# Optimization experiments

Measured on AMD Instinct MI355X. Metric: run time of the kernel, lower is better.

## Reference

```python
import jax, jax.numpy as jnp
import numpy as np

N_NODES = 50000
N_EDGES = 640000
IN_C, HID_C, OUT_C = 64, 128, 64


def _glorot(key, fan_in, fan_out):
    lim = float(np.sqrt(6.0 / (fan_in + fan_out)))
    return jax.random.uniform(key, (fan_in, fan_out), jnp.float32, -lim, lim)


def setup_inputs() -> dict:
    key = jax.random.key(0)
    ks = jax.random.split(key, 16)
    x = jax.random.normal(ks[0], (N_NODES, IN_C), jnp.float32)
    edge_index = jax.random.randint(ks[1], (2, N_EDGES), 0, N_NODES, jnp.int64)
    # SAGEConv params: out = mean_aggr(x_j) @ Wl + x @ Wr + b
    dims = [(IN_C, HID_C), (HID_C, HID_C), (HID_C, OUT_C)]
    params = {}
    for i, (fi, fo) in enumerate(dims):
        params[f"Wl{i}"] = _glorot(ks[2 + 3 * i], fi, fo)
        params[f"Wr{i}"] = _glorot(ks[3 + 3 * i], fi, fo)
        params[f"b{i}"] = jnp.zeros((fo,), jnp.float32)
    # classifier: Linear(64,32) -> ReLU -> Linear(32,1) -> Sigmoid (dropout off in eval)
    params["Wc1"] = _glorot(ks[11], OUT_C, 32)
    params["bc1"] = jnp.zeros((32,), jnp.float32)
    params["Wc2"] = _glorot(ks[12], 32, 1)
    params["bc2"] = jnp.zeros((1,), jnp.float32)
    return {"x": x, "edge_index": edge_index, **params}


def _sage_conv(x, src, dst, Wl, Wr, b):
    # gather neighbor (source) features along edges, mean-aggregate at target
    msgs = x[src]                                                    # [E, C]
    agg = jax.ops.segment_sum(msgs, dst, num_segments=N_NODES)      # [N, C]
    deg = jax.ops.segment_sum(jnp.ones((src.shape[0], 1), x.dtype), dst,
                              num_segments=N_NODES)                 # [N, 1]
    agg = agg / jnp.maximum(deg, 1.0)
    return agg @ Wl + x @ Wr + b


def reference(x, edge_index, Wl0, Wr0, b0, Wl1, Wr1, b1, Wl2, Wr2, b2,
              Wc1, bc1, Wc2, bc2):
    src, dst = edge_index[0], edge_index[1]
    h = jax.nn.relu(_sage_conv(x, src, dst, Wl0, Wr0, b0))
    h = jax.nn.relu(_sage_conv(h, src, dst, Wl1, Wr1, b1))
    h = _sage_conv(h, src, dst, Wl2, Wr2, b2)                       # [N, 64]
    h = jax.nn.relu(h @ Wc1 + bc1)                                  # [N, 32]
    return jax.nn.sigmoid(h @ Wc2 + bc2)                            # [N, 1]
```

## Files before the change

### kernel.cpp

```cpp
#include <hip/hip_runtime.h>
#include <math.h>

#define NN 50000
#define NE 640000
#define CAP 64

typedef short short8 __attribute__((ext_vector_type(8)));
typedef float f32x4  __attribute__((ext_vector_type(4)));

__device__ __forceinline__ unsigned bfr(float f) {
    unsigned u = __float_as_uint(f);
    return (u + 0x7FFFu + ((u >> 16) & 1u)) >> 16;
}
__device__ __forceinline__ unsigned pk2(float a, float b) { return bfr(a) | (bfr(b) << 16); }
__device__ __forceinline__ float bflo(unsigned u) { return __uint_as_float(u << 16); }
__device__ __forceinline__ float bfhi(unsigned u) { return __uint_as_float(u & 0xFFFF0000u); }

__device__ __forceinline__ void packOne(const float* Wl, const float* Wr,
                                        unsigned short* wp, int idx,
                                        int CIN, int COUT) {
    int k = idx / COUT, n = idx % COUT;
    float v = (k < CIN) ? Wl[k * COUT + n] : Wr[(k - CIN) * COUT + n];
    int kt = k >> 5, quad = (k >> 3) & 3, j = k & 7;
    int nt = n >> 4, l16 = n & 15;
    int NT = COUT / 16;
    wp[(((kt * NT + nt) * 64) + quad * 16 + l16) * 8 + j] = (unsigned short)bfr(v);
}

__global__ __launch_bounds__(256) void
k_prep(const int* __restrict__ src, const int* __restrict__ dst,
       int* __restrict__ cnt, int* __restrict__ nbr,
       const float* __restrict__ x, unsigned* __restrict__ xb,
       const float* Wl0, const float* Wr0, const float* Wl1, const float* Wr1,
       const float* Wl2, const float* Wr2, const float* Wc1,
       unsigned short* wp0, unsigned short* wp1, unsigned short* wp2,
       unsigned short* wpc) {
    const int b = blockIdx.x, t = threadIdx.x;
    if (b < 2500) {
        int e = b * 256 + t;
        if (e < NE) {
            int d = dst[e];
            int p = atomicAdd(&cnt[d], 1);
            if (p < CAP) nbr[d * CAP + p] = src[e];
        }
    } else if (b < 5625) {
        int i = (b - 2500) * 256 + t;
        if (i < NN * 16) {
            float4 v = ((const float4*)x)[i];
            ((uint2*)xb)[i] = make_uint2(pk2(v.x, v.y), pk2(v.z, v.w));
        }
    } else {
        int idx = (b - 5625) * 256 + t;
        if (idx < 16384) {
            packOne(Wl0, Wr0, wp0, idx, 64, 128);
        } else if (idx < 49152) {
            packOne(Wl1, Wr1, wp1, idx - 16384, 128, 128);
        } else if (idx < 65536) {
            packOne(Wl2, Wr2, wp2, idx - 49152, 128, 64);
        } else if (idx < 67584) {
            packOne(Wc1, Wc1, wpc, idx - 65536, 64, 32);
        }
    }
}

template <int LOGC>
__global__ __launch_bounds__(256) void
k_aggregate(const unsigned* __restrict__ xu, const int* __restrict__ nbr,
            const int* __restrict__ cnt, unsigned* __restrict__ aggu, int N) {
    constexpr int RU = 1 << (LOGC - 1);
    constexpr int PC = RU / 16;
    const int gw   = (blockIdx.x * 256 + threadIdx.x) >> 6;
    const int lane = threadIdx.x & 63;
    const int qw = lane >> 4, l16 = lane & 15;
    if (gw >= N) return;
    const int deg = cnt[gw];
    const int m = (deg < CAP) ? deg : CAP;

    int idx = 0;
    if (lane < m) idx = nbr[gw * CAP + lane];

    float a[2 * PC] = {};

#pragma unroll 4
    for (int j = 0; j < m; j += 4) {
        const int n = __shfl(idx, (j + qw) & 63);
        const bool valid = (j + qw) < m;
        if (PC == 2) {
            const uint2 u = *(const uint2*)(xu + (size_t)n * RU + l16 * 2);
            if (valid) {
                a[0] += bflo(u.x); a[1] += bfhi(u.x);
                a[2] += bflo(u.y); a[3] += bfhi(u.y);
            }
        } else {
            const uint4 u = *(const uint4*)(xu + (size_t)n * RU + l16 * 4);
            if (valid) {
                a[0] += bflo(u.x); a[1] += bfhi(u.x);
                a[2] += bflo(u.y); a[3] += bfhi(u.y);
                a[4] += bflo(u.z); a[5] += bfhi(u.z);
                a[6] += bflo(u.w); a[7] += bfhi(u.w);
            }
        }
    }

#pragma unroll
    for (int c = 0; c < 2 * PC; ++c) {
        a[c] += __shfl_xor(a[c], 16);
        a[c] += __shfl_xor(a[c], 32);
    }

    if (qw == 0) {
        const float di = 1.0f / (float)((deg > 1) ? deg : 1);
        if (PC == 2) {
            uint2 o = make_uint2(pk2(a[0] * di, a[1] * di), pk2(a[2] * di, a[3] * di));
            *(uint2*)(aggu + (size_t)gw * RU + l16 * 2) = o;
        } else {
            uint4 o = make_uint4(pk2(a[0] * di, a[1] * di), pk2(a[2] * di, a[3] * di),
                                 pk2(a[4] * di, a[5] * di), pk2(a[6] * di, a[7] * di));
            *(uint4*)(aggu + (size_t)gw * RU + l16 * 4) = o;
        }
    }
}

template <int CIN, int COUT, bool RELU>
__global__ __launch_bounds__(256) void
k_mfma(const unsigned short* __restrict__ Agg, const unsigned short* __restrict__ X,
       const unsigned short* __restrict__ Wpack, const float* __restrict__ bias,
       unsigned short* __restrict__ outp, int N) {
    constexpr int KT = (2 * CIN) / 32;
    constexpr int NT = COUT / 16;

    __shared__ short Bs[KT * NT * 64 * 8];

    const int t = threadIdx.x;
    const int wave = t >> 6, lane = t & 63;
    const int quad = lane >> 4, l16 = lane & 15;

    constexpr int NCHUNK = KT * NT * 64;
    for (int i = t; i < NCHUNK; i += 256)
        *(uint4*)&Bs[i * 8] = ((const uint4*)Wpack)[i];
    __syncthreads();

    const int row_base = blockIdx.x * 128 + wave * 32;
    int r0 = row_base + l16;      if (r0 >= N) r0 = N - 1;
    int r1 = row_base + 16 + l16; if (r1 >= N) r1 = N - 1;

    f32x4 acc[2][NT] = {};

    for (int kt = 0; kt < KT; ++kt) {
        const unsigned short* P = (kt < KT / 2) ? Agg : X;
        const int kb = (kt < KT / 2) ? kt * 32 : kt * 32 - CIN;
        const short8 a0 = *(const short8*)(P + (size_t)r0 * CIN + kb + quad * 8);
        const short8 a1 = *(const short8*)(P + (size_t)r1 * CIN + kb + quad * 8);
#pragma unroll
        for (int nt = 0; nt < NT; ++nt) {
            const short8 bfrag = *(const short8*)&Bs[((kt * NT + nt) * 64 + lane) * 8];
            acc[0][nt] = __builtin_amdgcn_mfma_f32_16x16x32_bf16(a0, bfrag, acc[0][nt], 0, 0, 0);
            acc[1][nt] = __builtin_amdgcn_mfma_f32_16x16x32_bf16(a1, bfrag, acc[1][nt], 0, 0, 0);
        }
    }

#pragma unroll
    for (int nt = 0; nt < NT; ++nt) {
        const int col = nt * 16 + l16;
        const float bb = bias[col];
#pragma unroll
        for (int s = 0; s < 2; ++s) {
#pragma unroll
            for (int rg = 0; rg < 4; ++rg) {
                int row = row_base + s * 16 + quad * 4 + rg;
                if (row < N) {
                    float v = acc[s][nt][rg] + bb;
                    if (RELU) v = fmaxf(v, 0.f);
                    outp[(size_t)row * COUT + col] = (unsigned short)bfr(v);
                }
            }
        }
    }
}

__global__ __launch_bounds__(256) void
k_mfma_cls(const unsigned short* __restrict__ Agg, const unsigned short* __restrict__ X,
           const unsigned short* __restrict__ Wpack, const unsigned short* __restrict__ WpackC,
           const float* __restrict__ bias, const float* __restrict__ bc1,
           const float* __restrict__ Wc2, const float* __restrict__ bc2,
           float* __restrict__ out, int N) {
    constexpr int CIN = 128, COUT = 64;
    constexpr int KT = 8, NT = 4;

    __shared__ __align__(16) short Bs[KT * NT * 64 * 8];
    __shared__ __align__(16) short Wc1s[2 * 2 * 64 * 8];
    __shared__ __align__(16) short Hs[8 * 16 * 64];
    __shared__ float sW2[32], sbc1[32];

    const int t = threadIdx.x;
    const int wave = t >> 6, lane = t & 63;
    const int quad = lane >> 4, l16 = lane & 15;

    for (int i = t; i < KT * NT * 64; i += 256)
        *(uint4*)&Bs[i * 8] = ((const uint4*)Wpack)[i];
    if (t < 256) *(uint4*)&Wc1s[t * 8] = ((const uint4*)WpackC)[t];
    if (t < 32) { sW2[t] = Wc2[t]; sbc1[t] = bc1[t]; }
    __syncthreads();

    const int row_base = blockIdx.x * 128 + wave * 32;
    int r0 = row_base + l16;      if (r0 >= N) r0 = N - 1;
    int r1 = row_base + 16 + l16; if (r1 >= N) r1 = N - 1;

    f32x4 acc[2][NT] = {};

    for (int kt = 0; kt < KT; ++kt) {
        const unsigned short* P = (kt < KT / 2) ? Agg : X;
        const int kb = (kt < KT / 2) ? kt * 32 : kt * 32 - CIN;
        const short8 a0 = *(const short8*)(P + (size_t)r0 * CIN + kb + quad * 8);
        const short8 a1 = *(const short8*)(P + (size_t)r1 * CIN + kb + quad * 8);
#pragma unroll
        for (int nt = 0; nt < NT; ++nt) {
            const short8 bfrag = *(const short8*)&Bs[((kt * NT + nt) * 64 + lane) * 8];
            acc[0][nt] = __builtin_amdgcn_mfma_f32_16x16x32_bf16(a0, bfrag, acc[0][nt], 0, 0, 0);
            acc[1][nt] = __builtin_amdgcn_mfma_f32_16x16x32_bf16(a1, bfrag, acc[1][nt], 0, 0, 0);
        }
    }

#pragma unroll
    for (int nt = 0; nt < NT; ++nt) {
        const float bb = bias[nt * 16 + l16];
#pragma unroll
        for (int s = 0; s < 2; ++s)
#pragma unroll
            for (int rg = 0; rg < 4; ++rg)
                Hs[(wave * 2 + s) * 1024 + (quad * 4 + rg) * 64 + nt * 16 + l16] =
                    (unsigned short)bfr(acc[s][nt][rg] + bb);
    }
    __syncthreads();

    f32x4 sacc[2][2] = {};
#pragma unroll
    for (int s = 0; s < 2; ++s)
#pragma unroll
        for (int kt2 = 0; kt2 < 2; ++kt2) {
            const short8 af = *(const short8*)&Hs[(wave * 2 + s) * 1024 + l16 * 64 +
                                                  kt2 * 32 + quad * 8];
#pragma unroll
            for (int nt2 = 0; nt2 < 2; ++nt2) {
                const short8 bf = *(const short8*)&Wc1s[((kt2 * 2 + nt2) * 64 + lane) * 8];
                sacc[s][nt2] = __builtin_amdgcn_mfma_f32_16x16x32_bf16(af, bf, sacc[s][nt2], 0, 0, 0);
            }
        }

    const float b1a = sbc1[l16], b1b = sbc1[16 + l16];
    const float w2a = sW2[l16],  w2b = sW2[16 + l16];
    const float b2v = bc2[0];
#pragma unroll
    for (int s = 0; s < 2; ++s)
#pragma unroll
        for (int rg = 0; rg < 4; ++rg) {
            float p = fmaxf(sacc[s][0][rg] + b1a, 0.f) * w2a +
                      fmaxf(sacc[s][1][rg] + b1b, 0.f) * w2b;
#pragma unroll
            for (int off = 1; off < 16; off <<= 1) p += __shfl_xor(p, off);
            if (l16 == 0) {
                int row = row_base + s * 16 + quad * 4 + rg;
                if (row < N) out[row] = 1.0f / (1.0f + expf(-(p + b2v)));
            }
        }
}

extern "C" void kernel_launch(void* const* d_in, const int* in_sizes, int n_in,
                              void* d_out, int out_size, void* d_ws, size_t ws_size,
                              hipStream_t stream) {
    const float* x   = (const float*)d_in[0];
    const int*   ei  = (const int*)d_in[1];
    const int*   src = ei;
    const int*   dst = ei + NE;
    const float* Wl0 = (const float*)d_in[2];
    const float* Wr0 = (const float*)d_in[3];
    const float* b0  = (const float*)d_in[4];
    const float* Wl1 = (const float*)d_in[5];
    const float* Wr1 = (const float*)d_in[6];
    const float* b1  = (const float*)d_in[7];
    const float* Wl2 = (const float*)d_in[8];
    const float* Wr2 = (const float*)d_in[9];
    const float* b2  = (const float*)d_in[10];
    const float* Wc1 = (const float*)d_in[11];
    const float* bc1 = (const float*)d_in[12];
    const float* Wc2 = (const float*)d_in[13];
    const float* bc2 = (const float*)d_in[14];
    float* out = (float*)d_out;

    char*  ws   = (char*)d_ws;
    int*   cnt  = (int*)(ws);
    unsigned short* wp0 = (unsigned short*)(ws + (size_t)256 * 1024);
    unsigned short* wp1 = (unsigned short*)(ws + (size_t)352 * 1024);
    unsigned short* wp2 = (unsigned short*)(ws + (size_t)448 * 1024);
    unsigned short* wpc = (unsigned short*)(ws + (size_t)512 * 1024);
    int*   nbr  = (int*)(ws + (size_t)1 * (1 << 20));
    unsigned short* xb   = (unsigned short*)(ws + (size_t)16 * (1 << 20));
    unsigned short* aggb = (unsigned short*)(ws + (size_t)24 * (1 << 20));
    unsigned short* h0b  = (unsigned short*)(ws + (size_t)40 * (1 << 20));
    unsigned short* h1b  = (unsigned short*)(ws + (size_t)56 * (1 << 20));

    const int B = 256;
    const int AGG_GRID = (NN + 3) / 4;
    const int MFMA_GRID = (NN + 127) / 128;

    hipMemsetAsync(cnt, 0, (size_t)NN * sizeof(int), stream);
    k_prep<<<5889, B, 0, stream>>>(src, dst, cnt, nbr, x, (unsigned*)xb,
                                   Wl0, Wr0, Wl1, Wr1, Wl2, Wr2, Wc1,
                                   wp0, wp1, wp2, wpc);

    k_aggregate<6><<<AGG_GRID, B, 0, stream>>>((const unsigned*)xb, nbr, cnt,
                                               (unsigned*)aggb, NN);
    k_mfma<64, 128, true><<<MFMA_GRID, 256, 0, stream>>>(aggb, xb, wp0, b0, h0b, NN);

    k_aggregate<7><<<AGG_GRID, B, 0, stream>>>((const unsigned*)h0b, nbr, cnt,
                                               (unsigned*)aggb, NN);
    k_mfma<128, 128, true><<<MFMA_GRID, 256, 0, stream>>>(aggb, h0b, wp1, b1, h1b, NN);

    k_aggregate<7><<<AGG_GRID, B, 0, stream>>>((const unsigned*)h1b, nbr, cnt,
                                               (unsigned*)aggb, NN);
    k_mfma_cls<<<MFMA_GRID, 256, 0, stream>>>(aggb, h1b, wp2, wpc, b2, bc1, Wc2, bc2,
                                              out, NN);
}
```

Baseline: 239.3 us.

## Fuse neighbor aggregation into per-layer MFMA kernels via LDS staging

Each SAGE layer is now a single kernel: every block gathers and mean-aggregates neighbor features for its 128 nodes into a padded LDS tile, then runs the MFMA GEMM, reading the aggregated half from LDS and the self half from global memory. This removes three aggregate launches and the global write and reread of the aggregated buffer. Weight fragments are now read straight from global or L2 instead of being staged in LDS. The cost is much less parallelism in the gather: 391 blocks, each wave walking 32 nodes one after another, where before one wave handled one node. This risks exposing latency on a memory-bound gather.

```diff
diff --git a/kernel.cpp b/kernel.cpp
--- a/kernel.cpp
+++ b/kernel.cpp
@@ -63,97 +63,112 @@
     }
 }
 
-template <int LOGC>
-__global__ __launch_bounds__(256) void
-k_aggregate(const unsigned* __restrict__ xu, const int* __restrict__ nbr,
-            const int* __restrict__ cnt, unsigned* __restrict__ aggu, int N) {
-    constexpr int RU = 1 << (LOGC - 1);
-    constexpr int PC = RU / 16;
-    const int gw   = (blockIdx.x * 256 + threadIdx.x) >> 6;
-    const int lane = threadIdx.x & 63;
-    const int qw = lane >> 4, l16 = lane & 15;
-    if (gw >= N) return;
-    const int deg = cnt[gw];
-    const int m = (deg < CAP) ? deg : CAP;
-
-    int idx = 0;
-    if (lane < m) idx = nbr[gw * CAP + lane];
-
-    float a[2 * PC] = {};
-
+template <int CIN, int RPAD>
+__device__ __forceinline__ void
+gather_to_lds(short* As, const unsigned short* __restrict__ Xprev,
+              const int* __restrict__ nbr, const int* __restrict__ cnt,
+              int nb0, int N, int wave, int lane, int qw, int l16) {
+    constexpr int PC = CIN / 32;
+    const unsigned* xu = (const unsigned*)Xprev;
+
+    int node = nb0 + wave * 32; if (node >= N) node = N - 1;
+    int dcur = cnt[node];
+    int scur = nbr[node * CAP + lane];
+
+    for (int it = 0; it < 32; ++it) {
+        const int deg = dcur;
+        const int sl  = scur;
+        if (it + 1 < 32) {
+            int nn = nb0 + wave * 32 + it + 1; if (nn >= N) nn = N - 1;
+            dcur = cnt[nn];
+            scur = nbr[nn * CAP + lane];
+        }
+        const int m = (deg < CAP) ? deg : CAP;
+        const int sc = (lane < m) ? sl : 0;
+
+        float a[2 * PC] = {};
 #pragma unroll 4
-    for (int j = 0; j < m; j += 4) {
-        const int n = __shfl(idx, (j + qw) & 63);
-        const bool valid = (j + qw) < m;
-        if (PC == 2) {
-            const uint2 u = *(const uint2*)(xu + (size_t)n * RU + l16 * 2);
-            if (valid) {
-                a[0] += bflo(u.x); a[1] += bfhi(u.x);
-                a[2] += bflo(u.y); a[3] += bfhi(u.y);
-            }
-        } else {
-            const uint4 u = *(const uint4*)(xu + (size_t)n * RU + l16 * 4);
-            if (valid) {
-                a[0] += bflo(u.x); a[1] += bfhi(u.x);
-                a[2] += bflo(u.y); a[3] += bfhi(u.y);
-                a[4] += bflo(u.z); a[5] += bfhi(u.z);
-                a[6] += bflo(u.w); a[7] += bfhi(u.w);
-            }
-        }
-    }
-
-#pragma unroll
-    for (int c = 0; c < 2 * PC; ++c) {
-        a[c] += __shfl_xor(a[c], 16);
-        a[c] += __shfl_xor(a[c], 32);
-    }
-
-    if (qw == 0) {
-        const float di = 1.0f / (float)((deg > 1) ? deg : 1);
-        if (PC == 2) {
-            uint2 o = make_uint2(pk2(a[0] * di, a[1] * di), pk2(a[2] * di, a[3] * di));
-            *(uint2*)(aggu + (size_t)gw * RU + l16 * 2) = o;
-        } else {
-            uint4 o = make_uint4(pk2(a[0] * di, a[1] * di), pk2(a[2] * di, a[3] * di),
-                                 pk2(a[4] * di, a[5] * di), pk2(a[6] * di, a[7] * di));
-            *(uint4*)(aggu + (size_t)gw * RU + l16 * 4) = o;
+        for (int j = 0; j < m; j += 4) {
+            const int n = __shfl(sc, (j + qw) & 63);
+            const bool valid = (j + qw) < m;
+            if (PC == 2) {
+                const uint2 u = *(const uint2*)(xu + (size_t)n * 32 + l16 * 2);
+                if (valid) {
+                    a[0] += bflo(u.x); a[1] += bfhi(u.x);
+                    a[2] += bflo(u.y); a[3] += bfhi(u.y);
+                }
+            } else {
+                const uint4 u = *(const uint4*)(xu + (size_t)n * 64 + l16 * 4);
+                if (valid) {
+                    a[0] += bflo(u.x); a[1] += bfhi(u.x);
+                    a[2] += bflo(u.y); a[3] += bfhi(u.y);
+                    a[4] += bflo(u.z); a[5] += bfhi(u.z);
+                    a[6] += bflo(u.w); a[7] += bfhi(u.w);
+                }
+            }
+        }
+
+#pragma unroll
+        for (int c = 0; c < 2 * PC; ++c) {
+            a[c] += __shfl_xor(a[c], 16);
+            a[c] += __shfl_xor(a[c], 32);
+        }
+
+        if (qw == 0) {
+            const float di = 1.0f / (float)((deg > 1) ? deg : 1);
+            const int row = wave * 32 + it;
+            if (PC == 2) {
+                uint2 o = make_uint2(pk2(a[0] * di, a[1] * di), pk2(a[2] * di, a[3] * di));
+                *(uint2*)&As[row * RPAD + l16 * 4] = o;
+            } else {
+                uint4 o = make_uint4(pk2(a[0] * di, a[1] * di), pk2(a[2] * di, a[3] * di),
+                                     pk2(a[4] * di, a[5] * di), pk2(a[6] * di, a[7] * di));
+                *(uint4*)&As[row * RPAD + l16 * 8] = o;
+            }
         }
     }
 }
 
 template <int CIN, int COUT, bool RELU>
-__global__ __launch_bounds__(256) void
-k_mfma(const unsigned short* __restrict__ Agg, const unsigned short* __restrict__ X,
-       const unsigned short* __restrict__ Wpack, const float* __restrict__ bias,
-       unsigned short* __restrict__ outp, int N) {
+__global__ __launch_bounds__(256, 2) void
+k_layer(const unsigned short* __restrict__ Xprev, const int* __restrict__ nbr,
+        const int* __restrict__ cnt, const unsigned short* __restrict__ Wpack,
+        const float* __restrict__ bias, unsigned short* __restrict__ outp, int N) {
     constexpr int KT = (2 * CIN) / 32;
     constexpr int NT = COUT / 16;
-
-    __shared__ short Bs[KT * NT * 64 * 8];
-
-    const int t = threadIdx.x;
-    const int wave = t >> 6, lane = t & 63;
-    const int quad = lane >> 4, l16 = lane & 15;
-
-    constexpr int NCHUNK = KT * NT * 64;
-    for (int i = t; i < NCHUNK; i += 256)
-        *(uint4*)&Bs[i * 8] = ((const uint4*)Wpack)[i];
+    constexpr int RPAD = CIN + 10;
+
+    __shared__ __align__(16) short As[128 * RPAD];
+
+    const int t = threadIdx.x, wave = t >> 6, lane = t & 63;
+    const int qw = lane >> 4, l16 = lane & 15;
+    const int nb0 = blockIdx.x * 128;
+
+    gather_to_lds<CIN, RPAD>(As, Xprev, nbr, cnt, nb0, N, wave, lane, qw, l16);
     __syncthreads();
 
-    const int row_base = blockIdx.x * 128 + wave * 32;
-    int r0 = row_base + l16;      if (r0 >= N) r0 = N - 1;
-    int r1 = row_base + 16 + l16; if (r1 >= N) r1 = N - 1;
+    const int row_base = nb0 + wave * 32;
+    int r0g = row_base + l16;      if (r0g >= N) r0g = N - 1;
+    int r1g = row_base + 16 + l16; if (r1g >= N) r1g = N - 1;
+    const int l0 = wave * 32 + l16;
+    const int l1 = wave * 32 + 16 + l16;
 
     f32x4 acc[2][NT] = {};
 
     for (int kt = 0; kt < KT; ++kt) {
-        const unsigned short* P = (kt < KT / 2) ? Agg : X;
-        const int kb = (kt < KT / 2) ? kt * 32 : kt * 32 - CIN;
-        const short8 a0 = *(const short8*)(P + (size_t)r0 * CIN + kb + quad * 8);
-        const short8 a1 = *(const short8*)(P + (size_t)r1 * CIN + kb + quad * 8);
+        short8 a0, a1;
+        if (kt < KT / 2) {
+            const int kb = kt * 32 + qw * 8;
+            a0 = *(const short8*)&As[l0 * RPAD + kb];
+            a1 = *(const short8*)&As[l1 * RPAD + kb];
+        } else {
+            const int kb = kt * 32 - CIN + qw * 8;
+            a0 = *(const short8*)(Xprev + (size_t)r0g * CIN + kb);
+            a1 = *(const short8*)(Xprev + (size_t)r1g * CIN + kb);
+        }
 #pragma unroll
         for (int nt = 0; nt < NT; ++nt) {
-            const short8 bfrag = *(const short8*)&Bs[((kt * NT + nt) * 64 + lane) * 8];
+            const short8 bfrag = *(const short8*)(Wpack + (size_t)((kt * NT + nt) * 64 + lane) * 8);
             acc[0][nt] = __builtin_amdgcn_mfma_f32_16x16x32_bf16(a0, bfrag, acc[0][nt], 0, 0, 0);
             acc[1][nt] = __builtin_amdgcn_mfma_f32_16x16x32_bf16(a1, bfrag, acc[1][nt], 0, 0, 0);
         }
@@ -167,7 +182,7 @@
         for (int s = 0; s < 2; ++s) {
 #pragma unroll
             for (int rg = 0; rg < 4; ++rg) {
-                int row = row_base + s * 16 + quad * 4 + rg;
+                int row = row_base + s * 16 + qw * 4 + rg;
                 if (row < N) {
                     float v = acc[s][nt][rg] + bb;
                     if (RELU) v = fmaxf(v, 0.f);
@@ -178,44 +193,48 @@
     }
 }
 
-__global__ __launch_bounds__(256) void
-k_mfma_cls(const unsigned short* __restrict__ Agg, const unsigned short* __restrict__ X,
-           const unsigned short* __restrict__ Wpack, const unsigned short* __restrict__ WpackC,
-           const float* __restrict__ bias, const float* __restrict__ bc1,
-           const float* __restrict__ Wc2, const float* __restrict__ bc2,
-           float* __restrict__ out, int N) {
+__global__ __launch_bounds__(256, 2) void
+k_layer_cls(const unsigned short* __restrict__ Xprev, const int* __restrict__ nbr,
+            const int* __restrict__ cnt, const unsigned short* __restrict__ Wpack,
+            const unsigned short* __restrict__ WpackC, const float* __restrict__ bias,
+            const float* __restrict__ bc1, const float* __restrict__ Wc2,
+            const float* __restrict__ bc2, float* __restrict__ out, int N) {
     constexpr int CIN = 128, COUT = 64;
     constexpr int KT = 8, NT = 4;
-
-    __shared__ __align__(16) short Bs[KT * NT * 64 * 8];
-    __shared__ __align__(16) short Wc1s[2 * 2 * 64 * 8];
+    constexpr int RPAD = CIN + 10;
+
+    __shared__ __align__(16) short As[128 * RPAD];
     __shared__ __align__(16) short Hs[8 * 16 * 64];
-    __shared__ float sW2[32], sbc1[32];
-
-    const int t = threadIdx.x;
-    const int wave = t >> 6, lane = t & 63;
-    const int quad = lane >> 4, l16 = lane & 15;
-
-    for (int i = t; i < KT * NT * 64; i += 256)
-        *(uint4*)&Bs[i * 8] = ((const uint4*)Wpack)[i];
-    if (t < 256) *(uint4*)&Wc1s[t * 8] = ((const uint4*)WpackC)[t];
-    if (t < 32) { sW2[t] = Wc2[t]; sbc1[t] = bc1[t]; }
+
+    const int t = threadIdx.x, wave = t >> 6, lane = t & 63;
+    const int qw = lane >> 4, l16 = lane & 15;
+    const int nb0 = blockIdx.x * 128;
+
+    gather_to_lds<CIN, RPAD>(As, Xprev, nbr, cnt, nb0, N, wave, lane, qw, l16);
     __syncthreads();
 
-    const int row_base = blockIdx.x * 128 + wave * 32;
-    int r0 = row_base + l16;      if (r0 >= N) r0 = N - 1;
-    int r1 = row_base + 16 + l16; if (r1 >= N) r1 = N - 1;
+    const int row_base = nb0 + wave * 32;
+    int r0g = row_base + l16;      if (r0g >= N) r0g = N - 1;
+    int r1g = row_base + 16 + l16; if (r1g >= N) r1g = N - 1;
+    const int l0 = wave * 32 + l16;
+    const int l1 = wave * 32 + 16 + l16;
 
     f32x4 acc[2][NT] = {};
 
     for (int kt = 0; kt < KT; ++kt) {
-        const unsigned short* P = (kt < KT / 2) ? Agg : X;
-        const int kb = (kt < KT / 2) ? kt * 32 : kt * 32 - CIN;
-        const short8 a0 = *(const short8*)(P + (size_t)r0 * CIN + kb + quad * 8);
-        const short8 a1 = *(const short8*)(P + (size_t)r1 * CIN + kb + quad * 8);
+        short8 a0, a1;
+        if (kt < KT / 2) {
+            const int kb = kt * 32 + qw * 8;
+            a0 = *(const short8*)&As[l0 * RPAD + kb];
+            a1 = *(const short8*)&As[l1 * RPAD + kb];
+        } else {
+            const int kb = kt * 32 - CIN + qw * 8;
+            a0 = *(const short8*)(Xprev + (size_t)r0g * CIN + kb);
+            a1 = *(const short8*)(Xprev + (size_t)r1g * CIN + kb);
+        }
 #pragma unroll
         for (int nt = 0; nt < NT; ++nt) {
-            const short8 bfrag = *(const short8*)&Bs[((kt * NT + nt) * 64 + lane) * 8];
+            const short8 bfrag = *(const short8*)(Wpack + (size_t)((kt * NT + nt) * 64 + lane) * 8);
             acc[0][nt] = __builtin_amdgcn_mfma_f32_16x16x32_bf16(a0, bfrag, acc[0][nt], 0, 0, 0);
             acc[1][nt] = __builtin_amdgcn_mfma_f32_16x16x32_bf16(a1, bfrag, acc[1][nt], 0, 0, 0);
         }
@@ -228,7 +247,7 @@
         for (int s = 0; s < 2; ++s)
 #pragma unroll
             for (int rg = 0; rg < 4; ++rg)
-                Hs[(wave * 2 + s) * 1024 + (quad * 4 + rg) * 64 + nt * 16 + l16] =
+                Hs[(wave * 2 + s) * 1024 + (qw * 4 + rg) * 64 + nt * 16 + l16] =
                     (unsigned short)bfr(acc[s][nt][rg] + bb);
     }
     __syncthreads();
@@ -239,16 +258,16 @@
 #pragma unroll
         for (int kt2 = 0; kt2 < 2; ++kt2) {
             const short8 af = *(const short8*)&Hs[(wave * 2 + s) * 1024 + l16 * 64 +
-                                                  kt2 * 32 + quad * 8];
+                                                  kt2 * 32 + qw * 8];
 #pragma unroll
             for (int nt2 = 0; nt2 < 2; ++nt2) {
-                const short8 bf = *(const short8*)&Wc1s[((kt2 * 2 + nt2) * 64 + lane) * 8];
+                const short8 bf = *(const short8*)(WpackC + (size_t)((kt2 * 2 + nt2) * 64 + lane) * 8);
                 sacc[s][nt2] = __builtin_amdgcn_mfma_f32_16x16x32_bf16(af, bf, sacc[s][nt2], 0, 0, 0);
             }
         }
 
-    const float b1a = sbc1[l16], b1b = sbc1[16 + l16];
-    const float w2a = sW2[l16],  w2b = sW2[16 + l16];
+    const float b1a = bc1[l16], b1b = bc1[16 + l16];
+    const float w2a = Wc2[l16], w2b = Wc2[16 + l16];
     const float b2v = bc2[0];
 #pragma unroll
     for (int s = 0; s < 2; ++s)
@@ -259,7 +278,7 @@
 #pragma unroll
             for (int off = 1; off < 16; off <<= 1) p += __shfl_xor(p, off);
             if (l16 == 0) {
-                int row = row_base + s * 16 + quad * 4 + rg;
+                int row = row_base + s * 16 + qw * 4 + rg;
                 if (row < N) out[row] = 1.0f / (1.0f + expf(-(p + b2v)));
             }
         }
@@ -294,30 +313,20 @@
     unsigned short* wp2 = (unsigned short*)(ws + (size_t)448 * 1024);
     unsigned short* wpc = (unsigned short*)(ws + (size_t)512 * 1024);
     int*   nbr  = (int*)(ws + (size_t)1 * (1 << 20));
-    unsigned short* xb   = (unsigned short*)(ws + (size_t)16 * (1 << 20));
-    unsigned short* aggb = (unsigned short*)(ws + (size_t)24 * (1 << 20));
-    unsigned short* h0b  = (unsigned short*)(ws + (size_t)40 * (1 << 20));
-    unsigned short* h1b  = (unsigned short*)(ws + (size_t)56 * (1 << 20));
+    unsigned short* xb  = (unsigned short*)(ws + (size_t)16 * (1 << 20));
+    unsigned short* h0b = (unsigned short*)(ws + (size_t)24 * (1 << 20));
+    unsigned short* h1b = (unsigned short*)(ws + (size_t)40 * (1 << 20));
 
     const int B = 256;
-    const int AGG_GRID = (NN + 3) / 4;
-    const int MFMA_GRID = (NN + 127) / 128;
+    const int LAYER_GRID = (NN + 127) / 128;
 
     hipMemsetAsync(cnt, 0, (size_t)NN * sizeof(int), stream);
     k_prep<<<5889, B, 0, stream>>>(src, dst, cnt, nbr, x, (unsigned*)xb,
                                    Wl0, Wr0, Wl1, Wr1, Wl2, Wr2, Wc1,
                                    wp0, wp1, wp2, wpc);
 
-    k_aggregate<6><<<AGG_GRID, B, 0, stream>>>((const unsigned*)xb, nbr, cnt,
-                                               (unsigned*)aggb, NN);
-    k_mfma<64, 128, true><<<MFMA_GRID, 256, 0, stream>>>(aggb, xb, wp0, b0, h0b, NN);
-
-    k_aggregate<7><<<AGG_GRID, B, 0, stream>>>((const unsigned*)h0b, nbr, cnt,
-                                               (unsigned*)aggb, NN);
-    k_mfma<128, 128, true><<<MFMA_GRID, 256, 0, stream>>>(aggb, h0b, wp1, b1, h1b, NN);
-
-    k_aggregate<7><<<AGG_GRID, B, 0, stream>>>((const unsigned*)h1b, nbr, cnt,
-                                               (unsigned*)aggb, NN);
-    k_mfma_cls<<<MFMA_GRID, 256, 0, stream>>>(aggb, h1b, wp2, wpc, b2, bc1, Wc2, bc2,
+    k_layer<64, 128, true><<<LAYER_GRID, B, 0, stream>>>(xb, nbr, cnt, wp0, b0, h0b, NN);
+    k_layer<128, 128, true><<<LAYER_GRID, B, 0, stream>>>(h0b, nbr, cnt, wp1, b1, h1b, NN);
+    k_layer_cls<<<LAYER_GRID, B, 0, stream>>>(h1b, nbr, cnt, wp2, wpc, b2, bc1, Wc2, bc2,
                                               out, NN);
 }
```

New measurement: 339.9 us. 1.42x slower.

## Fuse all GNN stages into one persistent cooperative kernel with grid syncs

Applied to the files above, without the earlier changes.

Replaces the seven separate launches (prep, three aggregate and three MFMA stages) with a single persistent cooperative kernel that grid-strides over work and uses grid.sync between phases. The aim is to remove per-launch overhead and the tail gaps between dependent kernels. The weights are now read from global memory instead of being staged in LDS, both in the fused kernel and in the fallback kernels. The fused path also caps the grid at 2048 blocks, which limits how much parallelism the aggregation phases can use, and each grid.sync adds its own cost.

```diff
diff --git a/kernel.cpp b/kernel.cpp
--- a/kernel.cpp
+++ b/kernel.cpp
@@ -1,5 +1,8 @@
 #include <hip/hip_runtime.h>
+#include <hip/hip_cooperative_groups.h>
 #include <math.h>
+
+namespace cg = cooperative_groups;
 
 #define NN 50000
 #define NE 640000
@@ -25,6 +28,240 @@
     int nt = n >> 4, l16 = n & 15;
     int NT = COUT / 16;
     wp[(((kt * NT + nt) * 64) + quad * 16 + l16) * 8 + j] = (unsigned short)bfr(v);
+}
+
+template <int LOGC>
+__device__ __forceinline__ void
+agg_phase(const unsigned* __restrict__ xu, const int* __restrict__ nbr,
+          const int* __restrict__ cnt, unsigned* __restrict__ aggu,
+          int wgl, int nwave, int lane) {
+    constexpr int RU = 1 << (LOGC - 1);
+    constexpr int PC = RU / 16;
+    const int qw = lane >> 4, l16 = lane & 15;
+
+    for (int gw = wgl; gw < NN; gw += nwave) {
+        const int deg = cnt[gw];
+        const int m = (deg < CAP) ? deg : CAP;
+
+        int idx = 0;
+        if (lane < m) idx = nbr[gw * CAP + lane];
+
+        float a[2 * PC] = {};
+
+#pragma unroll 4
+        for (int j = 0; j < m; j += 4) {
+            const int n = __shfl(idx, (j + qw) & 63);
+            const bool valid = (j + qw) < m;
+            if (PC == 2) {
+                const uint2 u = *(const uint2*)(xu + (size_t)n * RU + l16 * 2);
+                if (valid) {
+                    a[0] += bflo(u.x); a[1] += bfhi(u.x);
+                    a[2] += bflo(u.y); a[3] += bfhi(u.y);
+                }
+            } else {
+                const uint4 u = *(const uint4*)(xu + (size_t)n * RU + l16 * 4);
+                if (valid) {
+                    a[0] += bflo(u.x); a[1] += bfhi(u.x);
+                    a[2] += bflo(u.y); a[3] += bfhi(u.y);
+                    a[4] += bflo(u.z); a[5] += bfhi(u.z);
+                    a[6] += bflo(u.w); a[7] += bfhi(u.w);
+                }
+            }
+        }
+
+#pragma unroll
+        for (int c = 0; c < 2 * PC; ++c) {
+            a[c] += __shfl_xor(a[c], 16);
+            a[c] += __shfl_xor(a[c], 32);
+        }
+
+        if (qw == 0) {
+            const float di = 1.0f / (float)((deg > 1) ? deg : 1);
+            if (PC == 2) {
+                uint2 o = make_uint2(pk2(a[0] * di, a[1] * di), pk2(a[2] * di, a[3] * di));
+                *(uint2*)(aggu + (size_t)gw * RU + l16 * 2) = o;
+            } else {
+                uint4 o = make_uint4(pk2(a[0] * di, a[1] * di), pk2(a[2] * di, a[3] * di),
+                                     pk2(a[4] * di, a[5] * di), pk2(a[6] * di, a[7] * di));
+                *(uint4*)(aggu + (size_t)gw * RU + l16 * 4) = o;
+            }
+        }
+    }
+}
+
+template <int CIN, int COUT, bool RELU>
+__device__ __forceinline__ void
+mfma_phase(const unsigned short* __restrict__ Agg, const unsigned short* __restrict__ X,
+           const unsigned short* __restrict__ Wpack, const float* __restrict__ bias,
+           unsigned short* __restrict__ outp, int blk, int gstride, int wave, int lane) {
+    constexpr int KT = (2 * CIN) / 32;
+    constexpr int NT = COUT / 16;
+    const int quad = lane >> 4, l16 = lane & 15;
+    const int NTILE = (NN + 127) / 128;
+
+    for (int tile = blk; tile < NTILE; tile += gstride) {
+        const int row_base = tile * 128 + wave * 32;
+        int r0 = row_base + l16;      if (r0 >= NN) r0 = NN - 1;
+        int r1 = row_base + 16 + l16; if (r1 >= NN) r1 = NN - 1;
+
+        f32x4 acc[2][NT] = {};
+
+        for (int kt = 0; kt < KT; ++kt) {
+            const unsigned short* P = (kt < KT / 2) ? Agg : X;
+            const int kb = (kt < KT / 2) ? kt * 32 : kt * 32 - CIN;
+            const short8 a0 = *(const short8*)(P + (size_t)r0 * CIN + kb + quad * 8);
+            const short8 a1 = *(const short8*)(P + (size_t)r1 * CIN + kb + quad * 8);
+#pragma unroll
+            for (int nt = 0; nt < NT; ++nt) {
+                const short8 bfrag = *(const short8*)(Wpack + (size_t)((kt * NT + nt) * 64 + lane) * 8);
+                acc[0][nt] = __builtin_amdgcn_mfma_f32_16x16x32_bf16(a0, bfrag, acc[0][nt], 0, 0, 0);
+                acc[1][nt] = __builtin_amdgcn_mfma_f32_16x16x32_bf16(a1, bfrag, acc[1][nt], 0, 0, 0);
+            }
+        }
+
+#pragma unroll
+        for (int nt = 0; nt < NT; ++nt) {
+            const int col = nt * 16 + l16;
+            const float bb = bias[col];
+#pragma unroll
+            for (int s = 0; s < 2; ++s) {
+#pragma unroll
+                for (int rg = 0; rg < 4; ++rg) {
+                    int row = row_base + s * 16 + quad * 4 + rg;
+                    if (row < NN) {
+                        float v = acc[s][nt][rg] + bb;
+                        if (RELU) v = fmaxf(v, 0.f);
+                        outp[(size_t)row * COUT + col] = (unsigned short)bfr(v);
+                    }
+                }
+            }
+        }
+    }
+}
+
+__global__ __launch_bounds__(256) void
+k_all(const int* __restrict__ src, const int* __restrict__ dst,
+      const float* __restrict__ x,
+      const float* Wl0, const float* Wr0, const float* b0,
+      const float* Wl1, const float* Wr1, const float* b1,
+      const float* Wl2, const float* Wr2, const float* b2,
+      const float* Wc1, const float* bc1, const float* Wc2, const float* bc2,
+      int* cnt, int* nbr, unsigned short* xb,
+      unsigned short* wp0, unsigned short* wp1, unsigned short* wp2,
+      unsigned short* wpc,
+      unsigned short* aggb, unsigned short* h0b, unsigned short* h1b,
+      float* out) {
+    cg::grid_group grid = cg::this_grid();
+
+    __shared__ __align__(16) short Hs[8 * 16 * 64];
+
+    const int t = threadIdx.x, b = blockIdx.x;
+    const int nthr = gridDim.x * 256;
+    const int nwave = nthr >> 6;
+    const int gt = b * 256 + t;
+    const int wave = t >> 6, lane = t & 63;
+    const int wgl = gt >> 6;
+    const int quad = lane >> 4, l16 = lane & 15;
+
+    for (int e = gt; e < NE; e += nthr) {
+        int d = dst[e];
+        int p = atomicAdd(&cnt[d], 1);
+        if (p < CAP) nbr[d * CAP + p] = src[e];
+    }
+    for (int i = gt; i < NN * 16; i += nthr) {
+        float4 v = ((const float4*)x)[i];
+        ((uint2*)xb)[i] = make_uint2(pk2(v.x, v.y), pk2(v.z, v.w));
+    }
+    for (int i = gt; i < 67584; i += nthr) {
+        if (i < 16384) packOne(Wl0, Wr0, wp0, i, 64, 128);
+        else if (i < 49152) packOne(Wl1, Wr1, wp1, i - 16384, 128, 128);
+        else if (i < 65536) packOne(Wl2, Wr2, wp2, i - 49152, 128, 64);
+        else packOne(Wc1, Wc1, wpc, i - 65536, 64, 32);
+    }
+    grid.sync();
+
+    agg_phase<6>((const unsigned*)xb, nbr, cnt, (unsigned*)aggb, wgl, nwave, lane);
+    grid.sync();
+    mfma_phase<64, 128, true>(aggb, xb, wp0, b0, h0b, b, gridDim.x, wave, lane);
+    grid.sync();
+
+    agg_phase<7>((const unsigned*)h0b, nbr, cnt, (unsigned*)aggb, wgl, nwave, lane);
+    grid.sync();
+    mfma_phase<128, 128, true>(aggb, h0b, wp1, b1, h1b, b, gridDim.x, wave, lane);
+    grid.sync();
+
+    agg_phase<7>((const unsigned*)h1b, nbr, cnt, (unsigned*)aggb, wgl, nwave, lane);
+    grid.sync();
+
+    {
+        constexpr int CIN = 128, NT = 4, KT = 8;
+        const int NTILE = (NN + 127) / 128;
+
+        for (int tile = b; tile < NTILE; tile += gridDim.x) {
+            const int row_base = tile * 128 + wave * 32;
+            int r0 = row_base + l16;      if (r0 >= NN) r0 = NN - 1;
+            int r1 = row_base + 16 + l16; if (r1 >= NN) r1 = NN - 1;
+
+            f32x4 acc[2][NT] = {};
+
+            for (int kt = 0; kt < KT; ++kt) {
+                const unsigned short* P = (kt < KT / 2) ? aggb : h1b;
+                const int kb = (kt < KT / 2) ? kt * 32 : kt * 32 - CIN;
+                const short8 a0 = *(const short8*)(P + (size_t)r0 * CIN + kb + quad * 8);
+                const short8 a1 = *(const short8*)(P + (size_t)r1 * CIN + kb + quad * 8);
+#pragma unroll
+                for (int nt = 0; nt < NT; ++nt) {
+                    const short8 bfrag = *(const short8*)(wp2 + (size_t)((kt * NT + nt) * 64 + lane) * 8);
+                    acc[0][nt] = __builtin_amdgcn_mfma_f32_16x16x32_bf16(a0, bfrag, acc[0][nt], 0, 0, 0);
+                    acc[1][nt] = __builtin_amdgcn_mfma_f32_16x16x32_bf16(a1, bfrag, acc[1][nt], 0, 0, 0);
+                }
+            }
+
+#pragma unroll
+            for (int nt = 0; nt < NT; ++nt) {
+                const float bb = b2[nt * 16 + l16];
+#pragma unroll
+                for (int s = 0; s < 2; ++s)
+#pragma unroll
+                    for (int rg = 0; rg < 4; ++rg)
+                        Hs[(wave * 2 + s) * 1024 + (quad * 4 + rg) * 64 + nt * 16 + l16] =
+                            (unsigned short)bfr(acc[s][nt][rg] + bb);
+            }
+            __syncthreads();
+
+            f32x4 sacc[2][2] = {};
+#pragma unroll
+            for (int s = 0; s < 2; ++s)
+#pragma unroll
+                for (int kt2 = 0; kt2 < 2; ++kt2) {
+                    const short8 af = *(const short8*)&Hs[(wave * 2 + s) * 1024 + l16 * 64 +
+                                                          kt2 * 32 + quad * 8];
+#pragma unroll
+                    for (int nt2 = 0; nt2 < 2; ++nt2) {
+                        const short8 bf = *(const short8*)(wpc + (size_t)((kt2 * 2 + nt2) * 64 + lane) * 8);
+                        sacc[s][nt2] = __builtin_amdgcn_mfma_f32_16x16x32_bf16(af, bf, sacc[s][nt2], 0, 0, 0);
+                    }
+                }
+
+            const float b1a = bc1[l16], b1b = bc1[16 + l16];
+            const float w2a = Wc2[l16], w2b = Wc2[16 + l16];
+            const float b2v = bc2[0];
+#pragma unroll
+            for (int s = 0; s < 2; ++s)
+#pragma unroll
+                for (int rg = 0; rg < 4; ++rg) {
+                    float p = fmaxf(sacc[s][0][rg] + b1a, 0.f) * w2a +
+                              fmaxf(sacc[s][1][rg] + b1b, 0.f) * w2b;
+#pragma unroll
+                    for (int off = 1; off < 16; off <<= 1) p += __shfl_xor(p, off);
+                    if (l16 == 0) {
+                        int row = row_base + s * 16 + quad * 4 + rg;
+                        if (row < NN) out[row] = 1.0f / (1.0f + expf(-(p + b2v)));
+                    }
+                }
+            __syncthreads();
+        }
+    }
 }
 
 __global__ __launch_bounds__(256) void
@@ -51,15 +288,10 @@
         }
     } else {
         int idx = (b - 5625) * 256 + t;
-        if (idx < 16384) {
-            packOne(Wl0, Wr0, wp0, idx, 64, 128);
-        } else if (idx < 49152) {
-            packOne(Wl1, Wr1, wp1, idx - 16384, 128, 128);
-        } else if (idx < 65536) {
-            packOne(Wl2, Wr2, wp2, idx - 49152, 128, 64);
-        } else if (idx < 67584) {
-            packOne(Wc1, Wc1, wpc, idx - 65536, 64, 32);
-        }
+        if (idx < 16384) packOne(Wl0, Wr0, wp0, idx, 64, 128);
+        else if (idx < 49152) packOne(Wl1, Wr1, wp1, idx - 16384, 128, 128);
+        else if (idx < 65536) packOne(Wl2, Wr2, wp2, idx - 49152, 128, 64);
+        else if (idx < 67584) packOne(Wc1, Wc1, wpc, idx - 65536, 64, 32);
     }
 }
 
@@ -67,58 +299,9 @@
 __global__ __launch_bounds__(256) void
 k_aggregate(const unsigned* __restrict__ xu, const int* __restrict__ nbr,
             const int* __restrict__ cnt, unsigned* __restrict__ aggu, int N) {
-    constexpr int RU = 1 << (LOGC - 1);
-    constexpr int PC = RU / 16;
-    const int gw   = (blockIdx.x * 256 + threadIdx.x) >> 6;
-    const int lane = threadIdx.x & 63;
-    const int qw = lane >> 4, l16 = lane & 15;
-    if (gw >= N) return;
-    const int deg = cnt[gw];
-    const int m = (deg < CAP) ? deg : CAP;
-
-    int idx = 0;
-    if (lane < m) idx = nbr[gw * CAP + lane];
-
-    float a[2 * PC] = {};
-
-#pragma unroll 4
-    for (int j = 0; j < m; j += 4) {
-        const int n = __shfl(idx, (j + qw) & 63);
-        const bool valid = (j + qw) < m;
-        if (PC == 2) {
-            const uint2 u = *(const uint2*)(xu + (size_t)n * RU + l16 * 2);
-            if (valid) {
-                a[0] += bflo(u.x); a[1] += bfhi(u.x);
-                a[2] += bflo(u.y); a[3] += bfhi(u.y);
-            }
-        } else {
-            const uint4 u = *(const uint4*)(xu + (size_t)n * RU + l16 * 4);
-            if (valid) {
-                a[0] += bflo(u.x); a[1] += bfhi(u.x);
-                a[2] += bflo(u.y); a[3] += bfhi(u.y);
-                a[4] += bflo(u.z); a[5] += bfhi(u.z);
-                a[6] += bflo(u.w); a[7] += bfhi(u.w);
-            }
-        }
-    }
-
-#pragma unroll
-    for (int c = 0; c < 2 * PC; ++c) {
-        a[c] += __shfl_xor(a[c], 16);
-        a[c] += __shfl_xor(a[c], 32);
-    }
-
-    if (qw == 0) {
-        const float di = 1.0f / (float)((deg > 1) ? deg : 1);
-        if (PC == 2) {
-            uint2 o = make_uint2(pk2(a[0] * di, a[1] * di), pk2(a[2] * di, a[3] * di));
-            *(uint2*)(aggu + (size_t)gw * RU + l16 * 2) = o;
-        } else {
-            uint4 o = make_uint4(pk2(a[0] * di, a[1] * di), pk2(a[2] * di, a[3] * di),
-                                 pk2(a[4] * di, a[5] * di), pk2(a[6] * di, a[7] * di));
-            *(uint4*)(aggu + (size_t)gw * RU + l16 * 4) = o;
-        }
-    }
+    const int wgl = (blockIdx.x * 256 + threadIdx.x) >> 6;
+    if (wgl >= N) return;
+    agg_phase<LOGC>(xu, nbr, cnt, aggu, wgl, 1 << 30, threadIdx.x & 63);
 }
 
 template <int CIN, int COUT, bool RELU>
@@ -126,56 +309,8 @@
 k_mfma(const unsigned short* __restrict__ Agg, const unsigned short* __restrict__ X,
        const unsigned short* __restrict__ Wpack, const float* __restrict__ bias,
        unsigned short* __restrict__ outp, int N) {
-    constexpr int KT = (2 * CIN) / 32;
-    constexpr int NT = COUT / 16;
-
-    __shared__ short Bs[KT * NT * 64 * 8];
-
-    const int t = threadIdx.x;
-    const int wave = t >> 6, lane = t & 63;
-    const int quad = lane >> 4, l16 = lane & 15;
-
-    constexpr int NCHUNK = KT * NT * 64;
-    for (int i = t; i < NCHUNK; i += 256)
-        *(uint4*)&Bs[i * 8] = ((const uint4*)Wpack)[i];
-    __syncthreads();
-
-    const int row_base = blockIdx.x * 128 + wave * 32;
-    int r0 = row_base + l16;      if (r0 >= N) r0 = N - 1;
-    int r1 = row_base + 16 + l16; if (r1 >= N) r1 = N - 1;
-
-    f32x4 acc[2][NT] = {};
-
-    for (int kt = 0; kt < KT; ++kt) {
-        const unsigned short* P = (kt < KT / 2) ? Agg : X;
-        const int kb = (kt < KT / 2) ? kt * 32 : kt * 32 - CIN;
-        const short8 a0 = *(const short8*)(P + (size_t)r0 * CIN + kb + quad * 8);
-        const short8 a1 = *(const short8*)(P + (size_t)r1 * CIN + kb + quad * 8);
-#pragma unroll
-        for (int nt = 0; nt < NT; ++nt) {
-            const short8 bfrag = *(const short8*)&Bs[((kt * NT + nt) * 64 + lane) * 8];
-            acc[0][nt] = __builtin_amdgcn_mfma_f32_16x16x32_bf16(a0, bfrag, acc[0][nt], 0, 0, 0);
-            acc[1][nt] = __builtin_amdgcn_mfma_f32_16x16x32_bf16(a1, bfrag, acc[1][nt], 0, 0, 0);
-        }
-    }
-
-#pragma unroll
-    for (int nt = 0; nt < NT; ++nt) {
-        const int col = nt * 16 + l16;
-        const float bb = bias[col];
-#pragma unroll
-        for (int s = 0; s < 2; ++s) {
-#pragma unroll
-            for (int rg = 0; rg < 4; ++rg) {
-                int row = row_base + s * 16 + quad * 4 + rg;
-                if (row < N) {
-                    float v = acc[s][nt][rg] + bb;
-                    if (RELU) v = fmaxf(v, 0.f);
-                    outp[(size_t)row * COUT + col] = (unsigned short)bfr(v);
-                }
-            }
-        }
-    }
+    mfma_phase<CIN, COUT, RELU>(Agg, X, Wpack, bias, outp,
+                                blockIdx.x, 1 << 30, threadIdx.x >> 6, threadIdx.x & 63);
 }
 
 __global__ __launch_bounds__(256) void
@@ -184,23 +319,13 @@
            const float* __restrict__ bias, const float* __restrict__ bc1,
            const float* __restrict__ Wc2, const float* __restrict__ bc2,
            float* __restrict__ out, int N) {
-    constexpr int CIN = 128, COUT = 64;
-    constexpr int KT = 8, NT = 4;
-
-    __shared__ __align__(16) short Bs[KT * NT * 64 * 8];
-    __shared__ __align__(16) short Wc1s[2 * 2 * 64 * 8];
+    constexpr int CIN = 128, NT = 4, KT = 8;
+
     __shared__ __align__(16) short Hs[8 * 16 * 64];
-    __shared__ float sW2[32], sbc1[32];
 
     const int t = threadIdx.x;
     const int wave = t >> 6, lane = t & 63;
     const int quad = lane >> 4, l16 = lane & 15;
-
-    for (int i = t; i < KT * NT * 64; i += 256)
-        *(uint4*)&Bs[i * 8] = ((const uint4*)Wpack)[i];
-    if (t < 256) *(uint4*)&Wc1s[t * 8] = ((const uint4*)WpackC)[t];
-    if (t < 32) { sW2[t] = Wc2[t]; sbc1[t] = bc1[t]; }
-    __syncthreads();
 
     const int row_base = blockIdx.x * 128 + wave * 32;
     int r0 = row_base + l16;      if (r0 >= N) r0 = N - 1;
@@ -215,7 +340,7 @@
         const short8 a1 = *(const short8*)(P + (size_t)r1 * CIN + kb + quad * 8);
 #pragma unroll
         for (int nt = 0; nt < NT; ++nt) {
-            const short8 bfrag = *(const short8*)&Bs[((kt * NT + nt) * 64 + lane) * 8];
+            const short8 bfrag = *(const short8*)(Wpack + (size_t)((kt * NT + nt) * 64 + lane) * 8);
             acc[0][nt] = __builtin_amdgcn_mfma_f32_16x16x32_bf16(a0, bfrag, acc[0][nt], 0, 0, 0);
             acc[1][nt] = __builtin_amdgcn_mfma_f32_16x16x32_bf16(a1, bfrag, acc[1][nt], 0, 0, 0);
         }
@@ -242,13 +367,13 @@
                                                   kt2 * 32 + quad * 8];
 #pragma unroll
             for (int nt2 = 0; nt2 < 2; ++nt2) {
-                const short8 bf = *(const short8*)&Wc1s[((kt2 * 2 + nt2) * 64 + lane) * 8];
+                const short8 bf = *(const short8*)(WpackC + (size_t)((kt2 * 2 + nt2) * 64 + lane) * 8);
                 sacc[s][nt2] = __builtin_amdgcn_mfma_f32_16x16x32_bf16(af, bf, sacc[s][nt2], 0, 0, 0);
             }
         }
 
-    const float b1a = sbc1[l16], b1b = sbc1[16 + l16];
-    const float w2a = sW2[l16],  w2b = sW2[16 + l16];
+    const float b1a = bc1[l16], b1b = bc1[16 + l16];
+    const float w2a = Wc2[l16], w2b = Wc2[16 + l16];
     const float b2v = bc2[0];
 #pragma unroll
     for (int s = 0; s < 2; ++s)
@@ -299,25 +424,57 @@
     unsigned short* h0b  = (unsigned short*)(ws + (size_t)40 * (1 << 20));
     unsigned short* h1b  = (unsigned short*)(ws + (size_t)56 * (1 << 20));
 
-    const int B = 256;
-    const int AGG_GRID = (NN + 3) / 4;
-    const int MFMA_GRID = (NN + 127) / 128;
-
     hipMemsetAsync(cnt, 0, (size_t)NN * sizeof(int), stream);
-    k_prep<<<5889, B, 0, stream>>>(src, dst, cnt, nbr, x, (unsigned*)xb,
-                                   Wl0, Wr0, Wl1, Wr1, Wl2, Wr2, Wc1,
-                                   wp0, wp1, wp2, wpc);
-
-    k_aggregate<6><<<AGG_GRID, B, 0, stream>>>((const unsigned*)xb, nbr, cnt,
-                                               (unsigned*)aggb, NN);
-    k_mfma<64, 128, true><<<MFMA_GRID, 256, 0, stream>>>(aggb, xb, wp0, b0, h0b, NN);
-
-    k_aggregate<7><<<AGG_GRID, B, 0, stream>>>((const unsigned*)h0b, nbr, cnt,
-                                               (unsigned*)aggb, NN);
-    k_mfma<128, 128, true><<<MFMA_GRID, 256, 0, stream>>>(aggb, h0b, wp1, b1, h1b, NN);
-
-    k_aggregate<7><<<AGG_GRID, B, 0, stream>>>((const unsigned*)h1b, nbr, cnt,
-                                               (unsigned*)aggb, NN);
-    k_mfma_cls<<<MFMA_GRID, 256, 0, stream>>>(aggb, h1b, wp2, wpc, b2, bc1, Wc2, bc2,
-                                              out, NN);
-}
+
+    bool coop_ok = false;
+    int maxBpc = 0, ncu = 0, dev = 0;
+    hipGetDevice(&dev);
+    hipDeviceGetAttribute(&ncu, hipDeviceAttributeMultiprocessorCount, dev);
+    hipError_t qerr = hipOccupancyMaxActiveBlocksPerMultiprocessor(
+        &maxBpc, (const void*)k_all, 256, 0);
+    if (qerr == hipSuccess && maxBpc > 0 && ncu > 0) {
+        int grid = maxBpc * ncu;
+        if (grid > 2048) grid = 2048;
+        const int* srcp = src; const int* dstp = dst;
+        void* args[] = {
+            (void*)&srcp, (void*)&dstp, (void*)&x,
+            (void*)&Wl0, (void*)&Wr0, (void*)&b0,
+            (void*)&Wl1, (void*)&Wr1, (void*)&b1,
+            (void*)&Wl2, (void*)&Wr2, (void*)&b2,
+            (void*)&Wc1, (void*)&bc1, (void*)&Wc2, (void*)&bc2,
+            (void*)&cnt, (void*)&nbr, (void*)&xb,
+            (void*)&wp0, (void*)&wp1, (void*)&wp2, (void*)&wpc,
+            (void*)&aggb, (void*)&h0b, (void*)&h1b,
+            (void*)&out
+        };
+        hipError_t lerr = hipLaunchCooperativeKernel((const void*)k_all, dim3(grid),
+                                                     dim3(256), args, 0, stream);
+        if (lerr == hipSuccess) coop_ok = true;
+        else (void)hipGetLastError();
+    } else {
+        (void)hipGetLastError();
+    }
+
+    if (!coop_ok) {
+        const int B = 256;
+        const int AGG_GRID = (NN + 3) / 4;
+        const int MFMA_GRID = (NN + 127) / 128;
+
+        k_prep<<<5889, B, 0, stream>>>(src, dst, cnt, nbr, x, (unsigned*)xb,
+                                       Wl0, Wr0, Wl1, Wr1, Wl2, Wr2, Wc1,
+                                       wp0, wp1, wp2, wpc);
+
+        k_aggregate<6><<<AGG_GRID, B, 0, stream>>>((const unsigned*)xb, nbr, cnt,
+                                                   (unsigned*)aggb, NN);
+        k_mfma<64, 128, true><<<MFMA_GRID, B, 0, stream>>>(aggb, xb, wp0, b0, h0b, NN);
+
+        k_aggregate<7><<<AGG_GRID, B, 0, stream>>>((const unsigned*)h0b, nbr, cnt,
+                                                   (unsigned*)aggb, NN);
+        k_mfma<128, 128, true><<<MFMA_GRID, B, 0, stream>>>(aggb, h0b, wp1, b1, h1b, NN);
+
+        k_aggregate<7><<<AGG_GRID, B, 0, stream>>>((const unsigned*)h1b, nbr, cnt,
+                                                   (unsigned*)aggb, NN);
+        k_mfma_cls<<<MFMA_GRID, B, 0, stream>>>(aggb, h1b, wp2, wpc, b2, bc1, Wc2, bc2,
+                                                out, NN);
+    }
+}
```

New measurement: 231.9 us. 3.1% less time.
